# Performance work log

Measured on AMD Instinct MI355X. Metric: run time of the kernel, lower is better.

The kernel has to match this reference:

```python
import jax, jax.numpy as jnp
import numpy as np

A = -0.75  # cubic convolution coefficient used by PyTorch bicubic


def cubic_weights(t):
    """t: fractional offset in [0,1). Returns (4, *t.shape) weights for taps at
    floor-1, floor, floor+1, floor+2 (Keys cubic convolution, a=-0.75)."""
    t2 = t * t
    s = 1.0 - t
    w1 = (A + 2.0) * t * t2 - (A + 3.0) * t2 + 1.0          # dist = t
    w2 = (A + 2.0) * s * s * s - (A + 3.0) * s * s + 1.0     # dist = 1-t
    u = 1.0 + t
    w0 = A * (u * (u * (u - 5.0) + 8.0) - 4.0)               # dist = 1+t
    v = 2.0 - t
    w3 = A * (v * (v * (v - 5.0) + 8.0) - 4.0)               # dist = 2-t
    return jnp.stack([w0, w1, w2, w3])


def _resize_last(x, n_out):
    """Bicubic 1D resize along the last axis, align_corners=True, border-clamped
    access (matches F.interpolate(mode='bicubic', align_corners=True))."""
    n_in = x.shape[-1]
    if n_in == n_out:
        return x
    src = jnp.arange(n_out, dtype=x.dtype) * ((n_in - 1) / (n_out - 1))
    i0 = jnp.floor(src).astype(jnp.int32)
    t = src - i0.astype(x.dtype)
    w = cubic_weights(t)  # (4, n_out)
    out = jnp.zeros(x.shape[:-1] + (n_out,), x.dtype)
    for k in range(4):
        idx = jnp.clip(i0 - 1 + k, 0, n_in - 1)
        out = out + jnp.take(x, idx, axis=-1) * w[k]
    return out


def bicubic_resize(x, h_out, w_out):
    """x: (b, h, w, c) -> (b, h_out, w_out, c); separable, align_corners=True."""
    x = jnp.moveaxis(_resize_last(jnp.moveaxis(x, 1, -1), h_out), -1, 1)
    x = jnp.moveaxis(_resize_last(jnp.moveaxis(x, 2, -1), w_out), -1, 2)
    return x


def grid_sample_bicubic_zeros(img, gx, gy):
    """img: (b,H,W); gx,gy: (b,h,w) normalized coords in [-1,1].
    Matches F.grid_sample(mode='bicubic', padding_mode='zeros', align_corners=True)."""
    b, H, W = img.shape
    ix = (gx + 1.0) * 0.5 * (W - 1)
    iy = (gy + 1.0) * 0.5 * (H - 1)
    ix0 = jnp.floor(ix)
    iy0 = jnp.floor(iy)
    wx = cubic_weights(ix - ix0)  # (4,b,h,w)
    wy = cubic_weights(iy - iy0)
    ix0 = ix0.astype(jnp.int32)
    iy0 = iy0.astype(jnp.int32)
    b_idx = jnp.arange(b)[:, None, None]
    out = jnp.zeros(gx.shape, img.dtype)
    for i in range(4):
        yy = iy0 - 1 + i
        ymask = (yy >= 0) & (yy < H)
        yc = jnp.clip(yy, 0, H - 1)
        for j in range(4):
            xx = ix0 - 1 + j
            mask = ymask & (xx >= 0) & (xx < W)
            xc = jnp.clip(xx, 0, W - 1)
            v = img[b_idx, yc, xc]
            out = out + wy[i] * wx[j] * jnp.where(mask, v, 0.0)
    return out


def setup_inputs() -> dict:
    key = jax.random.key(0)
    k1, k2 = jax.random.split(key)
    B = 8
    PH, PW = 1024, 1024
    CH, CW = 16, 16
    input_phantom = jax.random.normal(k1, (B, 1, PH, PW), dtype=jnp.float32)
    # learned warp control points; small shifts like a trained model would have
    shiftmap = jax.random.normal(k2, (B, CH, CW, 2), dtype=jnp.float32) * 0.05
    # mesh buffer: meshgrid('ij') of linspace(-1,1,PH) x linspace(-1,1,PW), stacked last
    ys = jnp.linspace(-1.0, 1.0, PH, dtype=jnp.float32)
    xs = jnp.linspace(-1.0, 1.0, PW, dtype=jnp.float32)
    my, mx = jnp.meshgrid(ys, xs, indexing='ij')
    mesh = jnp.stack([my, mx], axis=-1)[None]  # (1, PH, PW, 2)
    return {"input_phantom": input_phantom, "shiftmap": shiftmap, "mesh": mesh}


def reference(input_phantom, shiftmap, mesh):
    b, _, H, W = input_phantom.shape
    ph, pw = mesh.shape[1], mesh.shape[2]
    ch, cw = shiftmap.shape[1], shiftmap.shape[2]
    trans = (ch == 1 and cw == 1)
    if (not trans) and (ch != ph or cw != pw):
        sm = bicubic_resize(shiftmap, ph, pw)  # (b, ph, pw, 2)
    else:
        sm = shiftmap
    shift_mesh = mesh + sm  # broadcast to (b, ph, pw, 2); channel 0 = y, 1 = x
    # .flip(-1) means grid x = channel 1, grid y = channel 0
    gx = shift_mesh[..., 1]
    gy = shift_mesh[..., 0]
    warped = grid_sample_bicubic_zeros(input_phantom[:, 0], gx, gy)
    return warped[:, None]  # (b, 1, ph, pw)
```

## Files before the change

kernel.cpp:

```cpp
#include <hip/hip_runtime.h>


static constexpr float A = -0.75f;
static constexpr int NXCD = 8;

typedef float f4u __attribute__((ext_vector_type(4), aligned(4)));

__device__ __forceinline__ void cubic_weights(float t, float* w) {
    float t2 = t * t;
    float s  = 1.0f - t;
    w[1] = (A + 2.0f) * t * t2 - (A + 3.0f) * t2 + 1.0f;
    w[2] = (A + 2.0f) * s * s * s - (A + 3.0f) * s * s + 1.0f;
    float u = 1.0f + t;
    w[0] = A * (u * (u * (u - 5.0f) + 8.0f) - 4.0f);
    w[3] = 1.0f - w[0] - w[1] - w[2];
}

template <int PX>
__global__ __launch_bounds__(256) void shiftmap_warp_kernel(
    const float* __restrict__ img,
    const float* __restrict__ smap,
    float* __restrict__ out,
    int H, int W, int CH, int CW, int nblocks)
{
    const int d   = blockIdx.x;
    const int per = nblocks / NXCD;
    const int work = (d % NXCD) * per + d / NXCD;
    const int y = work % H;
    const int b = work / H;
    const int tid = threadIdx.x;

    __shared__ float s_row[40];

    const float scale_y = (float)((double)(CH - 1) / (double)(H - 1));
    const float scale_x = (float)((double)(CW - 1) / (double)(W - 1));

    if (tid < 38) {
        const int c  = (tid >> 1) - 1;
        const int cc = min(max(c, 0), CW - 1);
        const int ch = tid & 1;
        const float sy  = y * scale_y;
        const float fy0 = floorf(sy);
        const int   cy0 = (int)fy0;
        float wy[4];
        cubic_weights(sy - fy0, wy);
        float v = 0.0f;
        #pragma unroll
        for (int i = 0; i < 4; ++i) {
            const int cy = min(max(cy0 - 1 + i, 0), CH - 1);
            v += wy[i] * smap[(((size_t)b * CH + cy) * CW + cc) * 2 + ch];
        }
        s_row[tid] = v;
    }
    __syncthreads();

    const float half_w = 0.5f * (float)(W - 1);
    const float half_h = 0.5f * (float)(H - 1);
    const float* imgb = img + (size_t)b * H * W;
    float* outb = out + (size_t)b * H * W + (size_t)y * W;

    #pragma unroll
    for (int k = 0; k < PX; ++k) {
        const int x = tid + k * 256;

        const float sx  = x * scale_x;
        const float fx0 = floorf(sx);
        const int   cx0 = (int)fx0;
        float wx[4];
        cubic_weights(sx - fx0, wx);
        const float* sr = s_row + cx0 * 2;
        const float smy = wx[0] * sr[0] + wx[1] * sr[2] + wx[2] * sr[4] + wx[3] * sr[6];
        const float smx = wx[0] * sr[1] + wx[1] * sr[3] + wx[2] * sr[5] + wx[3] * sr[7];

        const float ix = (float)x + smx * half_w;
        const float iy = (float)y + smy * half_h;
        const float ixf = floorf(ix), iyf = floorf(iy);
        const int ix0 = (int)ixf, iy0 = (int)iyf;
        float gwx[4], gwy[4];
        cubic_weights(ix - ixf, gwx);
        cubic_weights(iy - iyf, gwy);

        float acc = 0.0f;
        if (__builtin_expect((ix0 >= 1) & (ix0 <= W - 3) &
                             (iy0 >= 1) & (iy0 <= H - 3), 1)) {
            const float* p = imgb + (size_t)(iy0 - 1) * W + (ix0 - 1);
            const f4u r0 = *reinterpret_cast<const f4u*>(p);
            const f4u r1 = *reinterpret_cast<const f4u*>(p + W);
            const f4u r2 = *reinterpret_cast<const f4u*>(p + 2 * W);
            const f4u r3 = *reinterpret_cast<const f4u*>(p + 3 * W);
            acc  = gwy[0] * (gwx[0] * r0.x + gwx[1] * r0.y + gwx[2] * r0.z + gwx[3] * r0.w);
            acc += gwy[1] * (gwx[0] * r1.x + gwx[1] * r1.y + gwx[2] * r1.z + gwx[3] * r1.w);
            acc += gwy[2] * (gwx[0] * r2.x + gwx[1] * r2.y + gwx[2] * r2.z + gwx[3] * r2.w);
            acc += gwy[3] * (gwx[0] * r3.x + gwx[1] * r3.y + gwx[2] * r3.z + gwx[3] * r3.w);
        } else {
            #pragma unroll
            for (int i = 0; i < 4; ++i) {
                const int yy = iy0 - 1 + i;
                const bool vy = (yy >= 0) && (yy < H);
                const int yc = min(max(yy, 0), H - 1);
                const float* row = imgb + (size_t)yc * W;
                float r = 0.0f;
                #pragma unroll
                for (int j = 0; j < 4; ++j) {
                    const int xx = ix0 - 1 + j;
                    const bool v = vy && (xx >= 0) && (xx < W);
                    const int xc = min(max(xx, 0), W - 1);
                    r += gwx[j] * (v ? row[xc] : 0.0f);
                }
                acc += gwy[i] * r;
            }
        }
        outb[x] = acc;
    }
}

extern "C" void kernel_launch(void* const* d_in, const int* in_sizes, int n_in,
                              void* d_out, int out_size, void* d_ws, size_t ws_size,
                              hipStream_t stream) {
    const float* img  = (const float*)d_in[0];
    const float* smap = (const float*)d_in[1];
    float* out = (float*)d_out;

    const int H = 1024, W = 1024;
    const int CH = 16, CW = 16;
    const int B = in_sizes[0] / (H * W);
    const int nblocks = H * B;

    dim3 block(256);
    dim3 grid(nblocks);
    shiftmap_warp_kernel<4><<<grid, block, 0, stream>>>(img, smap, out,
                                                        H, W, CH, CW, nblocks);
}
```

Before: 48.26 us.

## Precompute x-axis cubic weights table and pack coordinate math into float2

Adds a small pre-kernel that writes per-column cubic interpolation weights for the shiftmap x-resize into workspace, so the main kernel loads them instead of recomputing them. The main kernel also pre-scales shared shiftmap values by half-width and half-height and swaps channels so the x/y math can use float2 packed operations. The cubic weight formula is refactored into a cheaper factored form. It keeps a fallback kernel for when workspace is too small, at the cost of an extra launch and a global table read per pixel.

Result: slower. 56.43 us (+16.9%).

```diff
diff --git a/kernel.cpp b/kernel.cpp
--- a/kernel.cpp
+++ b/kernel.cpp
@@ -5,23 +5,50 @@
 static constexpr int NXCD = 8;
 
 typedef float f4u __attribute__((ext_vector_type(4), aligned(4)));
+typedef float f4a __attribute__((ext_vector_type(4), aligned(16)));
+typedef float f2  __attribute__((ext_vector_type(2)));
 
 __device__ __forceinline__ void cubic_weights(float t, float* w) {
-    float t2 = t * t;
-    float s  = 1.0f - t;
-    w[1] = (A + 2.0f) * t * t2 - (A + 3.0f) * t2 + 1.0f;
-    w[2] = (A + 2.0f) * s * s * s - (A + 3.0f) * s * s + 1.0f;
-    float u = 1.0f + t;
-    w[0] = A * (u * (u * (u - 5.0f) + 8.0f) - 4.0f);
-    w[3] = 1.0f - w[0] - w[1] - w[2];
+    const float tm1 = t - 1.0f;
+    const float p   = t * tm1;
+    w[0] = (A * p) * tm1;
+    w[3] = (-A * p) * t;
+    const float t2 = t * t;
+    w[1] = (A + 2.0f) * t2 * t - (A + 3.0f) * t2 + 1.0f;
+    w[2] = 1.0f - w[0] - w[1] - w[3];
+}
+
+__device__ __forceinline__ void cubic_weights_pk(f2 t, f2* w) {
+    const f2 tm1 = t - 1.0f;
+    const f2 p   = t * tm1;
+    w[0] = (A * p) * tm1;
+    w[3] = (-A * p) * t;
+    const f2 t2 = t * t;
+    w[1] = (A + 2.0f) * t2 * t - (A + 3.0f) * t2 + 1.0f;
+    w[2] = 1.0f - w[0] - w[1] - w[3];
+}
+
+__global__ __launch_bounds__(256) void wxtab_kernel(
+    f4a* __restrict__ tab, int W, float scale_x)
+{
+    const int x = blockIdx.x * 256 + threadIdx.x;
+    if (x >= W) return;
+    const float sx = x * scale_x;
+    const float t  = sx - floorf(sx);
+    float w[4];
+    cubic_weights(t, w);
+    f4a v; v.x = w[0]; v.y = w[1]; v.z = w[2]; v.w = w[3];
+    tab[x] = v;
 }
 
 template <int PX>
 __global__ __launch_bounds__(256) void shiftmap_warp_kernel(
     const float* __restrict__ img,
     const float* __restrict__ smap,
+    const f4a* __restrict__ wxtab,
     float* __restrict__ out,
-    int H, int W, int CH, int CW, int nblocks)
+    int H, int W, int CH, int CW, int nblocks,
+    float scale_y, float scale_x, float half_h, float half_w)
 {
     const int d   = blockIdx.x;
     const int per = nblocks / NXCD;
@@ -30,10 +57,7 @@
     const int b = work / H;
     const int tid = threadIdx.x;
 
-    __shared__ float s_row[40];
-
-    const float scale_y = (float)((double)(CH - 1) / (double)(H - 1));
-    const float scale_x = (float)((double)(CW - 1) / (double)(W - 1));
+    __shared__ __align__(16) float s_row[40];
 
     if (tid < 38) {
         const int c  = (tid >> 1) - 1;
@@ -50,6 +74,105 @@
             const int cy = min(max(cy0 - 1 + i, 0), CH - 1);
             v += wy[i] * smap[(((size_t)b * CH + cy) * CW + cc) * 2 + ch];
         }
+        const float scale = ch ? half_w : half_h;
+        s_row[(c + 1) * 2 + (ch ^ 1)] = v * scale;
+    }
+    __syncthreads();
+
+    const f2* __restrict__ srow2 = reinterpret_cast<const f2*>(s_row);
+    const float* imgb = img + (size_t)b * H * W;
+    float* outb = out + (size_t)b * H * W + (size_t)y * W;
+
+    #pragma unroll
+    for (int k = 0; k < PX; ++k) {
+        const int x = tid + k * 256;
+
+        const f4a wxv = wxtab[x];
+        const int cx0 = (int)(x * scale_x);
+        const f2 c0 = srow2[cx0],     c1 = srow2[cx0 + 1],
+                 c2 = srow2[cx0 + 2], c3 = srow2[cx0 + 3];
+        const f2 sm = wxv.x * c0 + wxv.y * c1 + wxv.z * c2 + wxv.w * c3;
+
+        f2 xy; xy.x = (float)x; xy.y = (float)y;
+        const f2 pos = xy + sm;
+        const float ixf = floorf(pos.x), iyf = floorf(pos.y);
+        const int ix0 = (int)ixf, iy0 = (int)iyf;
+        f2 fl; fl.x = ixf; fl.y = iyf;
+        const f2 t = pos - fl;
+        f2 w0, w1, w2, w3;
+        {
+            f2 ww[4];
+            cubic_weights_pk(t, ww);
+            w0 = ww[0]; w1 = ww[1]; w2 = ww[2]; w3 = ww[3];
+        }
+
+        float acc = 0.0f;
+        if (__builtin_expect((ix0 >= 1) & (ix0 <= W - 3) &
+                             (iy0 >= 1) & (iy0 <= H - 3), 1)) {
+            const float* p = imgb + (size_t)(iy0 - 1) * W + (ix0 - 1);
+            const f4u r0 = *reinterpret_cast<const f4u*>(p);
+            const f4u r1 = *reinterpret_cast<const f4u*>(p + W);
+            const f4u r2 = *reinterpret_cast<const f4u*>(p + 2 * W);
+            const f4u r3 = *reinterpret_cast<const f4u*>(p + 3 * W);
+            acc  = w0.y * (w0.x * r0.x + w1.x * r0.y + w2.x * r0.z + w3.x * r0.w);
+            acc += w1.y * (w0.x * r1.x + w1.x * r1.y + w2.x * r1.z + w3.x * r1.w);
+            acc += w2.y * (w0.x * r2.x + w1.x * r2.y + w2.x * r2.z + w3.x * r2.w);
+            acc += w3.y * (w0.x * r3.x + w1.x * r3.y + w2.x * r3.z + w3.x * r3.w);
+        } else {
+            const float gwx[4] = {w0.x, w1.x, w2.x, w3.x};
+            const float gwy[4] = {w0.y, w1.y, w2.y, w3.y};
+            #pragma unroll
+            for (int i = 0; i < 4; ++i) {
+                const int yy = iy0 - 1 + i;
+                const bool vy = (yy >= 0) && (yy < H);
+                const int yc = min(max(yy, 0), H - 1);
+                const float* row = imgb + (size_t)yc * W;
+                float r = 0.0f;
+                #pragma unroll
+                for (int j = 0; j < 4; ++j) {
+                    const int xx = ix0 - 1 + j;
+                    const bool v = vy && (xx >= 0) && (xx < W);
+                    const int xc = min(max(xx, 0), W - 1);
+                    r += gwx[j] * (v ? row[xc] : 0.0f);
+                }
+                acc += gwy[i] * r;
+            }
+        }
+        outb[x] = acc;
+    }
+}
+
+template <int PX>
+__global__ __launch_bounds__(256) void shiftmap_warp_fallback(
+    const float* __restrict__ img, const float* __restrict__ smap,
+    float* __restrict__ out, int H, int W, int CH, int CW, int nblocks)
+{
+    const int d   = blockIdx.x;
+    const int per = nblocks / NXCD;
+    const int work = (d % NXCD) * per + d / NXCD;
+    const int y = work % H;
+    const int b = work / H;
+    const int tid = threadIdx.x;
+
+    __shared__ float s_row[40];
+    const float scale_y = (float)((double)(CH - 1) / (double)(H - 1));
+    const float scale_x = (float)((double)(CW - 1) / (double)(W - 1));
+
+    if (tid < 38) {
+        const int c  = (tid >> 1) - 1;
+        const int cc = min(max(c, 0), CW - 1);
+        const int ch = tid & 1;
+        const float sy  = y * scale_y;
+        const float fy0 = floorf(sy);
+        const int   cy0 = (int)fy0;
+        float wy[4];
+        cubic_weights(sy - fy0, wy);
+        float v = 0.0f;
+        #pragma unroll
+        for (int i = 0; i < 4; ++i) {
+            const int cy = min(max(cy0 - 1 + i, 0), CH - 1);
+            v += wy[i] * smap[(((size_t)b * CH + cy) * CW + cc) * 2 + ch];
+        }
         s_row[tid] = v;
     }
     __syncthreads();
@@ -62,7 +185,6 @@
     #pragma unroll
     for (int k = 0; k < PX; ++k) {
         const int x = tid + k * 256;
-
         const float sx  = x * scale_x;
         const float fx0 = floorf(sx);
         const int   cx0 = (int)fx0;
@@ -71,7 +193,6 @@
         const float* sr = s_row + cx0 * 2;
         const float smy = wx[0] * sr[0] + wx[1] * sr[2] + wx[2] * sr[4] + wx[3] * sr[6];
         const float smx = wx[0] * sr[1] + wx[1] * sr[3] + wx[2] * sr[5] + wx[3] * sr[7];
-
         const float ix = (float)x + smx * half_w;
         const float iy = (float)y + smy * half_h;
         const float ixf = floorf(ix), iyf = floorf(iy);
@@ -79,10 +200,8 @@
         float gwx[4], gwy[4];
         cubic_weights(ix - ixf, gwx);
         cubic_weights(iy - iyf, gwy);
-
         float acc = 0.0f;
-        if (__builtin_expect((ix0 >= 1) & (ix0 <= W - 3) &
-                             (iy0 >= 1) & (iy0 <= H - 3), 1)) {
+        if ((ix0 >= 1) & (ix0 <= W - 3) & (iy0 >= 1) & (iy0 <= H - 3)) {
             const float* p = imgb + (size_t)(iy0 - 1) * W + (ix0 - 1);
             const f4u r0 = *reinterpret_cast<const f4u*>(p);
             const f4u r1 = *reinterpret_cast<const f4u*>(p + W);
@@ -126,8 +245,20 @@
     const int B = in_sizes[0] / (H * W);
     const int nblocks = H * B;
 
-    dim3 block(256);
-    dim3 grid(nblocks);
-    shiftmap_warp_kernel<4><<<grid, block, 0, stream>>>(img, smap, out,
-                                                        H, W, CH, CW, nblocks);
-}
+    const float scale_y = (float)((double)(CH - 1) / (double)(H - 1));
+    const float scale_x = (float)((double)(CW - 1) / (double)(W - 1));
+    const float half_h = 0.5f * (float)(H - 1);
+    const float half_w = 0.5f * (float)(W - 1);
+
+    const size_t ws_needed = (size_t)W * sizeof(f4a);
+    if (ws_size >= ws_needed) {
+        f4a* wxtab = (f4a*)d_ws;
+        wxtab_kernel<<<dim3((W + 255) / 256), 256, 0, stream>>>(wxtab, W, scale_x);
+        shiftmap_warp_kernel<4><<<dim3(nblocks), 256, 0, stream>>>(
+            img, smap, wxtab, out, H, W, CH, CW, nblocks,
+            scale_y, scale_x, half_h, half_w);
+    } else {
+        shiftmap_warp_fallback<4><<<dim3(nblocks), 256, 0, stream>>>(
+            img, smap, out, H, W, CH, CW, nblocks);
+    }
+}
```
